# Optimization experiments

Hardware: AMD Instinct MI355X
Metric: run time of the kernel (lower is better)

Reference implementation:

```python
import jax, jax.numpy as jnp
import numpy as np

STRIDE = 32
WINDOW = 16


def setup_inputs() -> dict:
    key = jax.random.key(0)
    kq, kk, kv = jax.random.split(key, 3)
    B, H, S, D = 1, 16, 2048, 64
    q = jax.random.normal(kq, (B, H, S, D), dtype=jnp.float32)
    k = jax.random.normal(kk, (B, H, S, D), dtype=jnp.float32)
    v = jax.random.normal(kv, (B, H, S, D), dtype=jnp.float32)
    return {"q": q, "k": k, "v": v}


def _strided_attention(q, k, v, stride=STRIDE, w=WINDOW):
    b, h, n, d = q.shape
    scale = jnp.asarray(1.0 / np.sqrt(d), dtype=q.dtype)

    # strided (global) tokens: indices 0, stride, 2*stride, ...  [S_str]
    str_idx = jnp.arange(0, n, stride)
    k_str = k[:, :, str_idx, :]  # [b,h,S_str,d]
    v_str = v[:, :, str_idx, :]

    # local window gather: token i attends to j in [i-w, i+w]  (L = 2w+1 slots)
    offs = jnp.arange(-w, w + 1)                      # [L]
    pos = jnp.arange(n)[:, None] + offs[None, :]      # [n, L]
    local_valid = (pos >= 0) & (pos < n)              # [n, L]
    pos_c = jnp.clip(pos, 0, n - 1)
    k_loc = k[:, :, pos_c, :]                         # [b,h,n,L,d]
    v_loc = v[:, :, pos_c, :]                         # [b,h,n,L,d]

    # In the original, strided keys are concatenated ONLY when start > 0,
    # i.e. when i > w (since strided_indices[0] == 0 is inside the window
    # whenever start == 0). Duplicates (strided token inside the local
    # window) are intentionally kept, matching torch.cat semantics.
    use_str = jnp.arange(n) > w                       # [n]

    sc_loc = jnp.einsum('bhnd,bhnld->bhnl', q, k_loc) * scale
    sc_loc = jnp.where(local_valid[None, None], sc_loc, -jnp.inf)
    sc_str = jnp.einsum('bhnd,bhsd->bhns', q, k_str) * scale
    sc_str = jnp.where(use_str[None, None, :, None], sc_str, -jnp.inf)

    L = offs.shape[0]
    attn = jax.nn.softmax(jnp.concatenate([sc_loc, sc_str], axis=-1), axis=-1)
    attn = jnp.nan_to_num(attn, nan=0.0)
    a_loc, a_str = attn[..., :L], attn[..., L:]

    out = jnp.einsum('bhnl,bhnld->bhnd', a_loc, v_loc) \
        + jnp.einsum('bhns,bhsd->bhnd', a_str, v_str)
    return out


def reference(q, k, v):
    return _strided_attention(q, k, v)
```

## Files before the change

kernel.cpp:

```cpp
#include <hip/hip_runtime.h>
#include <math.h>


typedef __attribute__((ext_vector_type(8))) short bf16x8;
typedef __attribute__((ext_vector_type(4))) float f32x4;

constexpr int H = 16, S = 2048, D = 64, W = 16;
constexpr int QB      = 64;
constexpr int NLOCROW = 96;
constexpr int NROWS   = 160;
constexpr int NT      = 10;
constexpr float SCALE = 0.125f;

constexpr int QSTR = 72;
constexpr int VSTR = 168;
constexpr int QHI  = 0;
constexpr int QLO  = QHI + QB * QSTR;
constexpr int KHI  = QLO + QB * QSTR;
constexpr int KLO  = KHI + NROWS * QSTR;
constexpr int VTB  = KHI;
constexpr int PB   = VTB + D * VSTR;
constexpr int LDS_U = KLO + NROWS * QSTR;

__device__ __forceinline__ ushort f2bf(float x) {
    union { float f; unsigned u; } t; t.f = x;
    unsigned r = t.u + 0x7fffu + ((t.u >> 16) & 1u);
    return (ushort)(r >> 16);
}
__device__ __forceinline__ float bf2f(ushort b) {
    union { float f; unsigned u; } t; t.u = ((unsigned)b) << 16;
    return t.f;
}
__device__ __forceinline__ int rowpos(int r, int n0) {
    if (r < NLOCROW) {
        int p = n0 - W + r;
        return p < 0 ? 0 : (p > S - 1 ? S - 1 : p);
    }
    return (r - NLOCROW) * 32;
}

__global__ __launch_bounds__(256, 2) void strided_attn_mfma(
    const float* __restrict__ q,
    const float* __restrict__ k,
    const float* __restrict__ v,
    float* __restrict__ out)
{
    __shared__ ushort lds[LDS_U];

    const int tid  = threadIdx.x;
    const int w    = tid >> 6;
    const int lane = tid & 63;
    const int h    = blockIdx.x >> 5;
    const int n0   = (blockIdx.x & 31) << 6;

    const float* __restrict__ qh = q + (size_t)(h * S) * D;
    const float* __restrict__ kh = k + (size_t)(h * S) * D;
    const float* __restrict__ vh = v + (size_t)(h * S) * D;

    const int ntask = (tid < 128) ? 3 : 2;
    float4 vreg[3][4];
#pragma unroll
    for (int tt = 0; tt < 3; ++tt) {
        if (tt < ntask) {
            const int t2 = tid + (tt << 8);
            const int rp = t2 % 80, ch = t2 / 80;
            const int p0 = rowpos(2 * rp,     n0);
            const int p1 = rowpos(2 * rp + 1, n0);
            const float* s0 = vh + (size_t)p0 * D + ch * 8;
            const float* s1 = vh + (size_t)p1 * D + ch * 8;
            vreg[tt][0] = *(const float4*)s0;
            vreg[tt][1] = *(const float4*)(s0 + 4);
            vreg[tt][2] = *(const float4*)s1;
            vreg[tt][3] = *(const float4*)(s1 + 4);
        }
    }

    for (int t = tid; t < 1792; t += 256) {
        int row, ch, dhi, dlo;
        const float* src;
        if (t < 512) {
            row = t >> 3; ch = t & 7;
            src = qh + (size_t)(n0 + row) * D + ch * 8;
            dhi = QHI + row * QSTR + ch * 8;
            dlo = QLO + row * QSTR + ch * 8;
        } else {
            const int u = t - 512;
            row = u >> 3; ch = u & 7;
            src = kh + (size_t)rowpos(row, n0) * D + ch * 8;
            dhi = KHI + row * QSTR + ch * 8;
            dlo = KLO + row * QSTR + ch * 8;
        }
        const float4 a = *(const float4*)src;
        const float4 b = *(const float4*)(src + 4);
        const float xs[8] = {a.x, a.y, a.z, a.w, b.x, b.y, b.z, b.w};
        union { bf16x8 v; ushort u[8]; } hi, lo;
#pragma unroll
        for (int j = 0; j < 8; ++j) {
            const ushort hb = f2bf(xs[j]);
            hi.u[j] = hb;
            lo.u[j] = f2bf(xs[j] - bf2f(hb));
        }
        *(bf16x8*)&lds[dhi] = hi.v;
        *(bf16x8*)&lds[dlo] = lo.v;
    }
    __syncthreads();

    const int band = w * 16;
    const int c = lane & 15;
    const int g = lane >> 4;
    const int abase = (band + c) * QSTR + g * 8;
    const bf16x8 aH0 = *(bf16x8*)&lds[QHI + abase];
    const bf16x8 aH1 = *(bf16x8*)&lds[QHI + abase + 32];
    const bf16x8 aL0 = *(bf16x8*)&lds[QLO + abase];
    const bf16x8 aL1 = *(bf16x8*)&lds[QLO + abase + 32];

    f32x4 acc[NT];
#pragma unroll
    for (int t = 0; t < NT; ++t) acc[t] = (f32x4){0.f, 0.f, 0.f, 0.f};

#pragma unroll
    for (int t = 0; t < NT; ++t) {
        const int kb = (t * 16 + c) * QSTR + g * 8;
        const bf16x8 bH0 = *(bf16x8*)&lds[KHI + kb];
        const bf16x8 bH1 = *(bf16x8*)&lds[KHI + kb + 32];
        const bf16x8 bL0 = *(bf16x8*)&lds[KLO + kb];
        const bf16x8 bL1 = *(bf16x8*)&lds[KLO + kb + 32];
        f32x4 a4 = acc[t];
        a4 = __builtin_amdgcn_mfma_f32_16x16x32_bf16(aH0, bH0, a4, 0, 0, 0);
        a4 = __builtin_amdgcn_mfma_f32_16x16x32_bf16(aH1, bH1, a4, 0, 0, 0);
        a4 = __builtin_amdgcn_mfma_f32_16x16x32_bf16(aL0, bH0, a4, 0, 0, 0);
        a4 = __builtin_amdgcn_mfma_f32_16x16x32_bf16(aL1, bH1, a4, 0, 0, 0);
        a4 = __builtin_amdgcn_mfma_f32_16x16x32_bf16(aH0, bL0, a4, 0, 0, 0);
        a4 = __builtin_amdgcn_mfma_f32_16x16x32_bf16(aH1, bL1, a4, 0, 0, 0);
        acc[t] = a4;
    }

    float pw[4][NT];
    float linv[4];
#pragma unroll
    for (int i = 0; i < 4; ++i) {
        const int qi = band + g * 4 + i;
        const int n  = n0 + qi;
        float s[NT];
#pragma unroll
        for (int t = 0; t < 6; ++t) {
            const int j = t * 16 + c;
            const bool ok = ((unsigned)(j - qi) <= 32u) &&
                            ((unsigned)(n0 - W + j) < (unsigned)S);
            s[t] = ok ? acc[t][i] * SCALE : -INFINITY;
        }
        const bool us = n > W;
#pragma unroll
        for (int t = 6; t < NT; ++t)
            s[t] = us ? acc[t][i] * SCALE : -INFINITY;

        float m = s[0];
#pragma unroll
        for (int t = 1; t < NT; ++t) m = fmaxf(m, s[t]);
        m = fmaxf(m, __shfl_xor(m, 1));
        m = fmaxf(m, __shfl_xor(m, 2));
        m = fmaxf(m, __shfl_xor(m, 4));
        m = fmaxf(m, __shfl_xor(m, 8));

        float l = 0.f;
#pragma unroll
        for (int t = 0; t < NT; ++t) { pw[i][t] = __expf(s[t] - m); l += pw[i][t]; }
        l += __shfl_xor(l, 1);
        l += __shfl_xor(l, 2);
        l += __shfl_xor(l, 4);
        l += __shfl_xor(l, 8);
        linv[i] = 1.0f / l;
    }

    __syncthreads();

#pragma unroll
    for (int i = 0; i < 4; ++i) {
        const int pb = PB + (band + g * 4 + i) * VSTR + c;
#pragma unroll
        for (int t = 0; t < NT; ++t) lds[pb + t * 16] = f2bf(pw[i][t]);
    }

#pragma unroll
    for (int tt = 0; tt < 3; ++tt) {
        if (tt < ntask) {
            const int t2 = tid + (tt << 8);
            const int rp = t2 % 80, ch = t2 / 80;
            const float r0[8] = {vreg[tt][0].x, vreg[tt][0].y, vreg[tt][0].z, vreg[tt][0].w,
                                 vreg[tt][1].x, vreg[tt][1].y, vreg[tt][1].z, vreg[tt][1].w};
            const float r1[8] = {vreg[tt][2].x, vreg[tt][2].y, vreg[tt][2].z, vreg[tt][2].w,
                                 vreg[tt][3].x, vreg[tt][3].y, vreg[tt][3].z, vreg[tt][3].w};
#pragma unroll
            for (int j = 0; j < 8; ++j) {
                const unsigned pk = (unsigned)f2bf(r0[j]) | ((unsigned)f2bf(r1[j]) << 16);
                *(unsigned*)&lds[VTB + (ch * 8 + j) * VSTR + 2 * rp] = pk;
            }
        }
    }
    __syncthreads();

    f32x4 o[4];
#pragma unroll
    for (int dt = 0; dt < 4; ++dt) o[dt] = (f32x4){0.f, 0.f, 0.f, 0.f};

#pragma unroll
    for (int kt = 0; kt < 5; ++kt) {
        const bf16x8 pa = *(bf16x8*)&lds[PB + (band + c) * VSTR + kt * 32 + g * 8];
#pragma unroll
        for (int dt = 0; dt < 4; ++dt) {
            const bf16x8 vb = *(bf16x8*)&lds[VTB + (dt * 16 + c) * VSTR + kt * 32 + g * 8];
            o[dt] = __builtin_amdgcn_mfma_f32_16x16x32_bf16(pa, vb, o[dt], 0, 0, 0);
        }
    }

#pragma unroll
    for (int i = 0; i < 4; ++i) {
        const int n = n0 + band + g * 4 + i;
        float* op = out + ((size_t)(h * S) + n) * D + c;
#pragma unroll
        for (int dt = 0; dt < 4; ++dt) op[dt * 16] = o[dt][i] * linv[i];
    }
}

extern "C" void kernel_launch(void* const* d_in, const int* in_sizes, int n_in,
                              void* d_out, int out_size, void* d_ws, size_t ws_size,
                              hipStream_t stream) {
    (void)in_sizes; (void)n_in; (void)d_ws; (void)ws_size; (void)out_size;
    const float* q = (const float*)d_in[0];
    const float* k = (const float*)d_in[1];
    const float* v = (const float*)d_in[2];
    float* out     = (float*)d_out;

    dim3 grid(H * (S / QB));
    dim3 block(256);
    strided_attn_mfma<<<grid, block, 0, stream>>>(q, k, v, out);
}
```

Baseline: 18.41 us.

## Halve query block, split keys across warps, drop K low-part MFMAs

Query blocks shrink from 64 to 32 rows, and the four warps become a 2x2 grid: query band by key half (local versus strided). Partial softmax max and sum are merged through a small shared-memory buffer. K is stored only as bf16 hi, which drops the hi*lo correction MFMAs. The PV product is split across warps by output dimension, block IDs are swizzled, and occupancy is raised to 4 blocks per CU. In exchange there is an extra barrier, more grid blocks that reload the strided K/V rows, and lower precision for QK scores.

```diff
diff --git a/kernel.cpp b/kernel.cpp
--- a/kernel.cpp
+++ b/kernel.cpp
@@ -6,21 +6,20 @@
 typedef __attribute__((ext_vector_type(4))) float f32x4;
 
 constexpr int H = 16, S = 2048, D = 64, W = 16;
-constexpr int QB      = 64;
-constexpr int NLOCROW = 96;
-constexpr int NROWS   = 160;
-constexpr int NT      = 10;
+constexpr int QB    = 32;
+constexpr int NLOC  = 64;
+constexpr int NROWS = 128;
 constexpr float SCALE = 0.125f;
 
 constexpr int QSTR = 72;
-constexpr int VSTR = 168;
+constexpr int VSTR = 136;
 constexpr int QHI  = 0;
 constexpr int QLO  = QHI + QB * QSTR;
-constexpr int KHI  = QLO + QB * QSTR;
-constexpr int KLO  = KHI + NROWS * QSTR;
-constexpr int VTB  = KHI;
-constexpr int PB   = VTB + D * VSTR;
-constexpr int LDS_U = KLO + NROWS * QSTR;
+constexpr int KB   = QLO + QB * QSTR;
+constexpr int VTB  = 0;
+constexpr int PBF  = VTB + D * VSTR;
+constexpr int MLB  = KB + NROWS * QSTR;
+constexpr int LDS_U = MLB + 256;
 
 __device__ __forceinline__ ushort f2bf(float x) {
     union { float f; unsigned u; } t; t.f = x;
@@ -32,193 +31,203 @@
     return t.f;
 }
 __device__ __forceinline__ int rowpos(int r, int n0) {
-    if (r < NLOCROW) {
+    if (r < NLOC) {
         int p = n0 - W + r;
         return p < 0 ? 0 : (p > S - 1 ? S - 1 : p);
     }
-    return (r - NLOCROW) * 32;
-}
-
-__global__ __launch_bounds__(256, 2) void strided_attn_mfma(
+    return (r - NLOC) * 32;
+}
+
+__global__ __launch_bounds__(256, 4) void strided_attn_mfma(
     const float* __restrict__ q,
     const float* __restrict__ k,
     const float* __restrict__ v,
     float* __restrict__ out)
 {
     __shared__ ushort lds[LDS_U];
+    float* ml = (float*)&lds[MLB];
 
     const int tid  = threadIdx.x;
     const int w    = tid >> 6;
     const int lane = tid & 63;
-    const int h    = blockIdx.x >> 5;
-    const int n0   = (blockIdx.x & 31) << 6;
+    const int wq   = w >> 1;
+    const int wk   = w & 1;
+    const int bid  = blockIdx.x;
+    const int swz  = (bid & 7) * 128 + (bid >> 3);
+    const int h    = swz >> 6;
+    const int n0   = (swz & 63) << 5;
 
     const float* __restrict__ qh = q + (size_t)(h * S) * D;
     const float* __restrict__ kh = k + (size_t)(h * S) * D;
     const float* __restrict__ vh = v + (size_t)(h * S) * D;
 
-    const int ntask = (tid < 128) ? 3 : 2;
-    float4 vreg[3][4];
-#pragma unroll
-    for (int tt = 0; tt < 3; ++tt) {
-        if (tt < ntask) {
-            const int t2 = tid + (tt << 8);
-            const int rp = t2 % 80, ch = t2 / 80;
-            const int p0 = rowpos(2 * rp,     n0);
-            const int p1 = rowpos(2 * rp + 1, n0);
-            const float* s0 = vh + (size_t)p0 * D + ch * 8;
-            const float* s1 = vh + (size_t)p1 * D + ch * 8;
-            vreg[tt][0] = *(const float4*)s0;
-            vreg[tt][1] = *(const float4*)(s0 + 4);
-            vreg[tt][2] = *(const float4*)s1;
-            vreg[tt][3] = *(const float4*)(s1 + 4);
-        }
-    }
-
-    for (int t = tid; t < 1792; t += 256) {
-        int row, ch, dhi, dlo;
-        const float* src;
-        if (t < 512) {
-            row = t >> 3; ch = t & 7;
-            src = qh + (size_t)(n0 + row) * D + ch * 8;
-            dhi = QHI + row * QSTR + ch * 8;
-            dlo = QLO + row * QSTR + ch * 8;
+    float4 vreg[2][4];
+#pragma unroll
+    for (int tt = 0; tt < 2; ++tt) {
+        const int tau = tid + (tt << 8);
+        const int rp = tau & 63, ch = tau >> 6;
+        const int p0 = rowpos(2 * rp,     n0);
+        const int p1 = rowpos(2 * rp + 1, n0);
+        const float* s0 = vh + (size_t)p0 * D + ch * 8;
+        const float* s1 = vh + (size_t)p1 * D + ch * 8;
+        vreg[tt][0] = *(const float4*)s0;
+        vreg[tt][1] = *(const float4*)(s0 + 4);
+        vreg[tt][2] = *(const float4*)s1;
+        vreg[tt][3] = *(const float4*)(s1 + 4);
+    }
+
+    for (int t = tid; t < 1280; t += 256) {
+        if (t < 256) {
+            const int row = t >> 3, ch = t & 7;
+            const float* src = qh + (size_t)(n0 + row) * D + ch * 8;
+            const float4 a = *(const float4*)src;
+            const float4 b = *(const float4*)(src + 4);
+            const float xs[8] = {a.x, a.y, a.z, a.w, b.x, b.y, b.z, b.w};
+            union { bf16x8 v; ushort u[8]; } hi, lo;
+#pragma unroll
+            for (int j = 0; j < 8; ++j) {
+                const ushort hb = f2bf(xs[j]);
+                hi.u[j] = hb;
+                lo.u[j] = f2bf(xs[j] - bf2f(hb));
+            }
+            *(bf16x8*)&lds[QHI + row * QSTR + ch * 8] = hi.v;
+            *(bf16x8*)&lds[QLO + row * QSTR + ch * 8] = lo.v;
         } else {
-            const int u = t - 512;
-            row = u >> 3; ch = u & 7;
-            src = kh + (size_t)rowpos(row, n0) * D + ch * 8;
-            dhi = KHI + row * QSTR + ch * 8;
-            dlo = KLO + row * QSTR + ch * 8;
-        }
-        const float4 a = *(const float4*)src;
-        const float4 b = *(const float4*)(src + 4);
-        const float xs[8] = {a.x, a.y, a.z, a.w, b.x, b.y, b.z, b.w};
-        union { bf16x8 v; ushort u[8]; } hi, lo;
-#pragma unroll
-        for (int j = 0; j < 8; ++j) {
-            const ushort hb = f2bf(xs[j]);
-            hi.u[j] = hb;
-            lo.u[j] = f2bf(xs[j] - bf2f(hb));
-        }
-        *(bf16x8*)&lds[dhi] = hi.v;
-        *(bf16x8*)&lds[dlo] = lo.v;
+            const int u = t - 256;
+            const int row = u >> 3, ch = u & 7;
+            const float* src = kh + (size_t)rowpos(row, n0) * D + ch * 8;
+            const float4 a = *(const float4*)src;
+            const float4 b = *(const float4*)(src + 4);
+            const float xs[8] = {a.x, a.y, a.z, a.w, b.x, b.y, b.z, b.w};
+            union { bf16x8 v; ushort u[8]; } hi;
+#pragma unroll
+            for (int j = 0; j < 8; ++j) hi.u[j] = f2bf(xs[j]);
+            *(bf16x8*)&lds[KB + row * QSTR + ch * 8] = hi.v;
+        }
     }
     __syncthreads();
 
-    const int band = w * 16;
     const int c = lane & 15;
     const int g = lane >> 4;
-    const int abase = (band + c) * QSTR + g * 8;
+    const int abase = (wq * 16 + c) * QSTR + g * 8;
     const bf16x8 aH0 = *(bf16x8*)&lds[QHI + abase];
     const bf16x8 aH1 = *(bf16x8*)&lds[QHI + abase + 32];
     const bf16x8 aL0 = *(bf16x8*)&lds[QLO + abase];
     const bf16x8 aL1 = *(bf16x8*)&lds[QLO + abase + 32];
 
-    f32x4 acc[NT];
-#pragma unroll
-    for (int t = 0; t < NT; ++t) acc[t] = (f32x4){0.f, 0.f, 0.f, 0.f};
-
-#pragma unroll
-    for (int t = 0; t < NT; ++t) {
-        const int kb = (t * 16 + c) * QSTR + g * 8;
-        const bf16x8 bH0 = *(bf16x8*)&lds[KHI + kb];
-        const bf16x8 bH1 = *(bf16x8*)&lds[KHI + kb + 32];
-        const bf16x8 bL0 = *(bf16x8*)&lds[KLO + kb];
-        const bf16x8 bL1 = *(bf16x8*)&lds[KLO + kb + 32];
+    f32x4 acc[4];
+#pragma unroll
+    for (int t = 0; t < 4; ++t) acc[t] = (f32x4){0.f, 0.f, 0.f, 0.f};
+#pragma unroll
+    for (int t = 0; t < 4; ++t) {
+        const int kb = KB + (wk * 64 + t * 16 + c) * QSTR + g * 8;
+        const bf16x8 b0 = *(bf16x8*)&lds[kb];
+        const bf16x8 b1 = *(bf16x8*)&lds[kb + 32];
         f32x4 a4 = acc[t];
-        a4 = __builtin_amdgcn_mfma_f32_16x16x32_bf16(aH0, bH0, a4, 0, 0, 0);
-        a4 = __builtin_amdgcn_mfma_f32_16x16x32_bf16(aH1, bH1, a4, 0, 0, 0);
-        a4 = __builtin_amdgcn_mfma_f32_16x16x32_bf16(aL0, bH0, a4, 0, 0, 0);
-        a4 = __builtin_amdgcn_mfma_f32_16x16x32_bf16(aL1, bH1, a4, 0, 0, 0);
-        a4 = __builtin_amdgcn_mfma_f32_16x16x32_bf16(aH0, bL0, a4, 0, 0, 0);
-        a4 = __builtin_amdgcn_mfma_f32_16x16x32_bf16(aH1, bL1, a4, 0, 0, 0);
+        a4 = __builtin_amdgcn_mfma_f32_16x16x32_bf16(aH0, b0, a4, 0, 0, 0);
+        a4 = __builtin_amdgcn_mfma_f32_16x16x32_bf16(aH1, b1, a4, 0, 0, 0);
+        a4 = __builtin_amdgcn_mfma_f32_16x16x32_bf16(aL0, b0, a4, 0, 0, 0);
+        a4 = __builtin_amdgcn_mfma_f32_16x16x32_bf16(aL1, b1, a4, 0, 0, 0);
         acc[t] = a4;
     }
 
-    float pw[4][NT];
-    float linv[4];
+    float sv[4][4];
+    float mw[4], lw[4];
 #pragma unroll
     for (int i = 0; i < 4; ++i) {
-        const int qi = band + g * 4 + i;
+        const int qi = wq * 16 + g * 4 + i;
         const int n  = n0 + qi;
-        float s[NT];
-#pragma unroll
-        for (int t = 0; t < 6; ++t) {
-            const int j = t * 16 + c;
-            const bool ok = ((unsigned)(j - qi) <= 32u) &&
-                            ((unsigned)(n0 - W + j) < (unsigned)S);
-            s[t] = ok ? acc[t][i] * SCALE : -INFINITY;
-        }
-        const bool us = n > W;
-#pragma unroll
-        for (int t = 6; t < NT; ++t)
-            s[t] = us ? acc[t][i] * SCALE : -INFINITY;
-
-        float m = s[0];
-#pragma unroll
-        for (int t = 1; t < NT; ++t) m = fmaxf(m, s[t]);
+        if (wk == 0) {
+#pragma unroll
+            for (int t = 0; t < 4; ++t) {
+                const int j = t * 16 + c;
+                const bool ok = ((unsigned)(j - qi) <= 32u) &&
+                                ((unsigned)(n0 - W + j) < (unsigned)S);
+                sv[i][t] = ok ? acc[t][i] * SCALE : -INFINITY;
+            }
+        } else {
+            const bool us = n > W;
+#pragma unroll
+            for (int t = 0; t < 4; ++t)
+                sv[i][t] = us ? acc[t][i] * SCALE : -INFINITY;
+        }
+        float m = fmaxf(fmaxf(sv[i][0], sv[i][1]), fmaxf(sv[i][2], sv[i][3]));
         m = fmaxf(m, __shfl_xor(m, 1));
         m = fmaxf(m, __shfl_xor(m, 2));
         m = fmaxf(m, __shfl_xor(m, 4));
         m = fmaxf(m, __shfl_xor(m, 8));
-
+        mw[i] = m;
+        const float ms = fmaxf(m, -1e30f);
         float l = 0.f;
 #pragma unroll
-        for (int t = 0; t < NT; ++t) { pw[i][t] = __expf(s[t] - m); l += pw[i][t]; }
+        for (int t = 0; t < 4; ++t) l += __expf(sv[i][t] - ms);
         l += __shfl_xor(l, 1);
         l += __shfl_xor(l, 2);
         l += __shfl_xor(l, 4);
         l += __shfl_xor(l, 8);
+        lw[i] = l;
+    }
+    if (c == 0) {
+#pragma unroll
+        for (int i = 0; i < 4; ++i) {
+            const int qi = wq * 16 + g * 4 + i;
+            ml[qi * 4 + wk * 2 + 0] = mw[i];
+            ml[qi * 4 + wk * 2 + 1] = lw[i];
+        }
+    }
+    __syncthreads();
+
+    float linv[4];
+#pragma unroll
+    for (int i = 0; i < 4; ++i) {
+        const int qi = wq * 16 + g * 4 + i;
+        const float m0 = ml[qi * 4 + 0], l0 = ml[qi * 4 + 1];
+        const float m1 = ml[qi * 4 + 2], l1 = ml[qi * 4 + 3];
+        const float m  = fmaxf(m0, m1);
+        const float l  = l0 * __expf(fmaxf(m0, -1e30f) - m)
+                       + l1 * __expf(fmaxf(m1, -1e30f) - m);
         linv[i] = 1.0f / l;
-    }
-
+        const int pb = PBF + qi * VSTR + wk * 64;
+#pragma unroll
+        for (int t = 0; t < 4; ++t)
+            lds[pb + t * 16 + c] = f2bf(__expf(sv[i][t] - m));
+    }
+
+#pragma unroll
+    for (int tt = 0; tt < 2; ++tt) {
+        const int tau = tid + (tt << 8);
+        const int rp = tau & 63, ch = tau >> 6;
+        const float r0[8] = {vreg[tt][0].x, vreg[tt][0].y, vreg[tt][0].z, vreg[tt][0].w,
+                             vreg[tt][1].x, vreg[tt][1].y, vreg[tt][1].z, vreg[tt][1].w};
+        const float r1[8] = {vreg[tt][2].x, vreg[tt][2].y, vreg[tt][2].z, vreg[tt][2].w,
+                             vreg[tt][3].x, vreg[tt][3].y, vreg[tt][3].z, vreg[tt][3].w};
+#pragma unroll
+        for (int j = 0; j < 8; ++j) {
+            const unsigned pk = (unsigned)f2bf(r0[j]) | ((unsigned)f2bf(r1[j]) << 16);
+            *(unsigned*)&lds[VTB + (ch * 8 + j) * VSTR + 2 * rp] = pk;
+        }
+    }
     __syncthreads();
 
+    f32x4 o[2];
+    o[0] = (f32x4){0.f, 0.f, 0.f, 0.f};
+    o[1] = (f32x4){0.f, 0.f, 0.f, 0.f};
+#pragma unroll
+    for (int kt = 0; kt < 4; ++kt) {
+        const bf16x8 pa = *(bf16x8*)&lds[PBF + (wq * 16 + c) * VSTR + kt * 32 + g * 8];
+#pragma unroll
+        for (int dt = 0; dt < 2; ++dt) {
+            const bf16x8 vb = *(bf16x8*)&lds[VTB + (wk * 32 + dt * 16 + c) * VSTR + kt * 32 + g * 8];
+            o[dt] = __builtin_amdgcn_mfma_f32_16x16x32_bf16(pa, vb, o[dt], 0, 0, 0);
+        }
+    }
+
 #pragma unroll
     for (int i = 0; i < 4; ++i) {
-        const int pb = PB + (band + g * 4 + i) * VSTR + c;
-#pragma unroll
-        for (int t = 0; t < NT; ++t) lds[pb + t * 16] = f2bf(pw[i][t]);
-    }
-
-#pragma unroll
-    for (int tt = 0; tt < 3; ++tt) {
-        if (tt < ntask) {
-            const int t2 = tid + (tt << 8);
-            const int rp = t2 % 80, ch = t2 / 80;
-            const float r0[8] = {vreg[tt][0].x, vreg[tt][0].y, vreg[tt][0].z, vreg[tt][0].w,
-                                 vreg[tt][1].x, vreg[tt][1].y, vreg[tt][1].z, vreg[tt][1].w};
-            const float r1[8] = {vreg[tt][2].x, vreg[tt][2].y, vreg[tt][2].z, vreg[tt][2].w,
-                                 vreg[tt][3].x, vreg[tt][3].y, vreg[tt][3].z, vreg[tt][3].w};
-#pragma unroll
-            for (int j = 0; j < 8; ++j) {
-                const unsigned pk = (unsigned)f2bf(r0[j]) | ((unsigned)f2bf(r1[j]) << 16);
-                *(unsigned*)&lds[VTB + (ch * 8 + j) * VSTR + 2 * rp] = pk;
-            }
-        }
-    }
-    __syncthreads();
-
-    f32x4 o[4];
-#pragma unroll
-    for (int dt = 0; dt < 4; ++dt) o[dt] = (f32x4){0.f, 0.f, 0.f, 0.f};
-
-#pragma unroll
-    for (int kt = 0; kt < 5; ++kt) {
-        const bf16x8 pa = *(bf16x8*)&lds[PB + (band + c) * VSTR + kt * 32 + g * 8];
-#pragma unroll
-        for (int dt = 0; dt < 4; ++dt) {
-            const bf16x8 vb = *(bf16x8*)&lds[VTB + (dt * 16 + c) * VSTR + kt * 32 + g * 8];
-            o[dt] = __builtin_amdgcn_mfma_f32_16x16x32_bf16(pa, vb, o[dt], 0, 0, 0);
-        }
-    }
-
-#pragma unroll
-    for (int i = 0; i < 4; ++i) {
-        const int n = n0 + band + g * 4 + i;
-        float* op = out + ((size_t)(h * S) + n) * D + c;
-#pragma unroll
-        for (int dt = 0; dt < 4; ++dt) op[dt * 16] = o[dt][i] * linv[i];
+        const int n = n0 + wq * 16 + g * 4 + i;
+        float* op = out + ((size_t)(h * S) + n) * D + wk * 32 + c;
+        op[0]  = o[0][i] * linv[i];
+        op[16] = o[1][i] * linv[i];
     }
 }
 
```

Result: faster. 17.88 us (-2.9%).

## Transpose QK^T so P stays in registers; drop K low split; swizzle blocks

Applied to the files above, without the earlier changes.

Computes S^T = K·Q^T so that each lane holds one query's scores. The softmax reduction then needs only two cross-lane shuffles, and the normalized probabilities can be packed directly into MFMA A-operands in registers instead of going through an LDS P buffer. The V^T layout is permuted so it matches that register ordering. The K low-precision split term is dropped, which cuts QK MFMAs from 6 to 4 per tile and halves K LDS storage, at some cost in score accuracy. A block-index swizzle is also added, and V conversion to bf16 is done before the barrier.

```diff
diff --git a/kernel.cpp b/kernel.cpp
--- a/kernel.cpp
+++ b/kernel.cpp
@@ -6,21 +6,19 @@
 typedef __attribute__((ext_vector_type(4))) float f32x4;
 
 constexpr int H = 16, S = 2048, D = 64, W = 16;
-constexpr int QB      = 64;
-constexpr int NLOCROW = 96;
-constexpr int NROWS   = 160;
-constexpr int NT      = 10;
+constexpr int QB    = 64;
+constexpr int NLOC  = 96;
+constexpr int NROWS = 160;
+constexpr int NT    = 10;
 constexpr float SCALE = 0.125f;
 
 constexpr int QSTR = 72;
 constexpr int VSTR = 168;
 constexpr int QHI  = 0;
 constexpr int QLO  = QHI + QB * QSTR;
-constexpr int KHI  = QLO + QB * QSTR;
-constexpr int KLO  = KHI + NROWS * QSTR;
-constexpr int VTB  = KHI;
-constexpr int PB   = VTB + D * VSTR;
-constexpr int LDS_U = KLO + NROWS * QSTR;
+constexpr int KB   = QLO + QB * QSTR;
+constexpr int VTB  = 0;
+constexpr int LDS_U = KB + NROWS * QSTR;
 
 __device__ __forceinline__ ushort f2bf(float x) {
     union { float f; unsigned u; } t; t.f = x;
@@ -31,12 +29,15 @@
     union { float f; unsigned u; } t; t.u = ((unsigned)b) << 16;
     return t.f;
 }
+__device__ __forceinline__ unsigned pk2(float a, float b) {
+    return (unsigned)f2bf(a) | ((unsigned)f2bf(b) << 16);
+}
 __device__ __forceinline__ int rowpos(int r, int n0) {
-    if (r < NLOCROW) {
+    if (r < NLOC) {
         int p = n0 - W + r;
         return p < 0 ? 0 : (p > S - 1 ? S - 1 : p);
     }
-    return (r - NLOCROW) * 32;
+    return (r - NLOC) * 32;
 }
 
 __global__ __launch_bounds__(256, 2) void strided_attn_mfma(
@@ -50,8 +51,12 @@
     const int tid  = threadIdx.x;
     const int w    = tid >> 6;
     const int lane = tid & 63;
-    const int h    = blockIdx.x >> 5;
-    const int n0   = (blockIdx.x & 31) << 6;
+    const int c    = lane & 15;
+    const int g    = lane >> 4;
+    const int bid  = blockIdx.x;
+    const int swz  = (bid & 7) * 64 + (bid >> 3);
+    const int h    = swz >> 5;
+    const int n0   = (swz & 31) << 6;
 
     const float* __restrict__ qh = q + (size_t)(h * S) * D;
     const float* __restrict__ kh = k + (size_t)(h * S) * D;
@@ -62,12 +67,10 @@
 #pragma unroll
     for (int tt = 0; tt < 3; ++tt) {
         if (tt < ntask) {
-            const int t2 = tid + (tt << 8);
-            const int rp = t2 % 80, ch = t2 / 80;
-            const int p0 = rowpos(2 * rp,     n0);
-            const int p1 = rowpos(2 * rp + 1, n0);
-            const float* s0 = vh + (size_t)p0 * D + ch * 8;
-            const float* s1 = vh + (size_t)p1 * D + ch * 8;
+            const int tau = tid + (tt << 8);
+            const int rp = tau % 80, ch = tau / 80;
+            const float* s0 = vh + (size_t)rowpos(2 * rp,     n0) * D + ch * 8;
+            const float* s1 = vh + (size_t)rowpos(2 * rp + 1, n0) * D + ch * 8;
             vreg[tt][0] = *(const float4*)s0;
             vreg[tt][1] = *(const float4*)(s0 + 4);
             vreg[tt][2] = *(const float4*)s1;
@@ -76,149 +79,153 @@
     }
 
     for (int t = tid; t < 1792; t += 256) {
-        int row, ch, dhi, dlo;
-        const float* src;
         if (t < 512) {
-            row = t >> 3; ch = t & 7;
-            src = qh + (size_t)(n0 + row) * D + ch * 8;
-            dhi = QHI + row * QSTR + ch * 8;
-            dlo = QLO + row * QSTR + ch * 8;
+            const int row = t >> 3, ch = t & 7;
+            const float* src = qh + (size_t)(n0 + row) * D + ch * 8;
+            const float4 a = *(const float4*)src;
+            const float4 b = *(const float4*)(src + 4);
+            const float xs[8] = {a.x, a.y, a.z, a.w, b.x, b.y, b.z, b.w};
+            union { bf16x8 v; ushort u[8]; } hi, lo;
+#pragma unroll
+            for (int j = 0; j < 8; ++j) {
+                const ushort hb = f2bf(xs[j]);
+                hi.u[j] = hb;
+                lo.u[j] = f2bf(xs[j] - bf2f(hb));
+            }
+            *(bf16x8*)&lds[QHI + row * QSTR + ch * 8] = hi.v;
+            *(bf16x8*)&lds[QLO + row * QSTR + ch * 8] = lo.v;
         } else {
             const int u = t - 512;
-            row = u >> 3; ch = u & 7;
-            src = kh + (size_t)rowpos(row, n0) * D + ch * 8;
-            dhi = KHI + row * QSTR + ch * 8;
-            dlo = KLO + row * QSTR + ch * 8;
-        }
-        const float4 a = *(const float4*)src;
-        const float4 b = *(const float4*)(src + 4);
-        const float xs[8] = {a.x, a.y, a.z, a.w, b.x, b.y, b.z, b.w};
-        union { bf16x8 v; ushort u[8]; } hi, lo;
-#pragma unroll
-        for (int j = 0; j < 8; ++j) {
-            const ushort hb = f2bf(xs[j]);
-            hi.u[j] = hb;
-            lo.u[j] = f2bf(xs[j] - bf2f(hb));
-        }
-        *(bf16x8*)&lds[dhi] = hi.v;
-        *(bf16x8*)&lds[dlo] = lo.v;
-    }
-    __syncthreads();
-
-    const int band = w * 16;
-    const int c = lane & 15;
-    const int g = lane >> 4;
-    const int abase = (band + c) * QSTR + g * 8;
-    const bf16x8 aH0 = *(bf16x8*)&lds[QHI + abase];
-    const bf16x8 aH1 = *(bf16x8*)&lds[QHI + abase + 32];
-    const bf16x8 aL0 = *(bf16x8*)&lds[QLO + abase];
-    const bf16x8 aL1 = *(bf16x8*)&lds[QLO + abase + 32];
-
-    f32x4 acc[NT];
-#pragma unroll
-    for (int t = 0; t < NT; ++t) acc[t] = (f32x4){0.f, 0.f, 0.f, 0.f};
-
-#pragma unroll
-    for (int t = 0; t < NT; ++t) {
-        const int kb = (t * 16 + c) * QSTR + g * 8;
-        const bf16x8 bH0 = *(bf16x8*)&lds[KHI + kb];
-        const bf16x8 bH1 = *(bf16x8*)&lds[KHI + kb + 32];
-        const bf16x8 bL0 = *(bf16x8*)&lds[KLO + kb];
-        const bf16x8 bL1 = *(bf16x8*)&lds[KLO + kb + 32];
-        f32x4 a4 = acc[t];
-        a4 = __builtin_amdgcn_mfma_f32_16x16x32_bf16(aH0, bH0, a4, 0, 0, 0);
-        a4 = __builtin_amdgcn_mfma_f32_16x16x32_bf16(aH1, bH1, a4, 0, 0, 0);
-        a4 = __builtin_amdgcn_mfma_f32_16x16x32_bf16(aL0, bH0, a4, 0, 0, 0);
-        a4 = __builtin_amdgcn_mfma_f32_16x16x32_bf16(aL1, bH1, a4, 0, 0, 0);
-        a4 = __builtin_amdgcn_mfma_f32_16x16x32_bf16(aH0, bL0, a4, 0, 0, 0);
-        a4 = __builtin_amdgcn_mfma_f32_16x16x32_bf16(aH1, bL1, a4, 0, 0, 0);
-        acc[t] = a4;
-    }
-
-    float pw[4][NT];
-    float linv[4];
-#pragma unroll
-    for (int i = 0; i < 4; ++i) {
-        const int qi = band + g * 4 + i;
-        const int n  = n0 + qi;
-        float s[NT];
-#pragma unroll
-        for (int t = 0; t < 6; ++t) {
-            const int j = t * 16 + c;
-            const bool ok = ((unsigned)(j - qi) <= 32u) &&
-                            ((unsigned)(n0 - W + j) < (unsigned)S);
-            s[t] = ok ? acc[t][i] * SCALE : -INFINITY;
-        }
-        const bool us = n > W;
-#pragma unroll
-        for (int t = 6; t < NT; ++t)
-            s[t] = us ? acc[t][i] * SCALE : -INFINITY;
-
-        float m = s[0];
-#pragma unroll
-        for (int t = 1; t < NT; ++t) m = fmaxf(m, s[t]);
-        m = fmaxf(m, __shfl_xor(m, 1));
-        m = fmaxf(m, __shfl_xor(m, 2));
-        m = fmaxf(m, __shfl_xor(m, 4));
-        m = fmaxf(m, __shfl_xor(m, 8));
-
-        float l = 0.f;
-#pragma unroll
-        for (int t = 0; t < NT; ++t) { pw[i][t] = __expf(s[t] - m); l += pw[i][t]; }
-        l += __shfl_xor(l, 1);
-        l += __shfl_xor(l, 2);
-        l += __shfl_xor(l, 4);
-        l += __shfl_xor(l, 8);
-        linv[i] = 1.0f / l;
-    }
-
-    __syncthreads();
-
-#pragma unroll
-    for (int i = 0; i < 4; ++i) {
-        const int pb = PB + (band + g * 4 + i) * VSTR + c;
-#pragma unroll
-        for (int t = 0; t < NT; ++t) lds[pb + t * 16] = f2bf(pw[i][t]);
-    }
-
+            const int row = u >> 3, ch = u & 7;
+            const float* src = kh + (size_t)rowpos(row, n0) * D + ch * 8;
+            const float4 a = *(const float4*)src;
+            const float4 b = *(const float4*)(src + 4);
+            const float xs[8] = {a.x, a.y, a.z, a.w, b.x, b.y, b.z, b.w};
+            union { bf16x8 v; ushort u[8]; } hi;
+#pragma unroll
+            for (int j = 0; j < 8; ++j) hi.u[j] = f2bf(xs[j]);
+            *(bf16x8*)&lds[KB + row * QSTR + ch * 8] = hi.v;
+        }
+    }
+
+    unsigned vpk[3][8];
 #pragma unroll
     for (int tt = 0; tt < 3; ++tt) {
         if (tt < ntask) {
-            const int t2 = tid + (tt << 8);
-            const int rp = t2 % 80, ch = t2 / 80;
             const float r0[8] = {vreg[tt][0].x, vreg[tt][0].y, vreg[tt][0].z, vreg[tt][0].w,
                                  vreg[tt][1].x, vreg[tt][1].y, vreg[tt][1].z, vreg[tt][1].w};
             const float r1[8] = {vreg[tt][2].x, vreg[tt][2].y, vreg[tt][2].z, vreg[tt][2].w,
                                  vreg[tt][3].x, vreg[tt][3].y, vreg[tt][3].z, vreg[tt][3].w};
 #pragma unroll
-            for (int j = 0; j < 8; ++j) {
-                const unsigned pk = (unsigned)f2bf(r0[j]) | ((unsigned)f2bf(r1[j]) << 16);
-                *(unsigned*)&lds[VTB + (ch * 8 + j) * VSTR + 2 * rp] = pk;
-            }
+            for (int j = 0; j < 8; ++j) vpk[tt][j] = pk2(r0[j], r1[j]);
         }
     }
     __syncthreads();
 
+    const int qb = w * 16;
+    const int qi = qb + c;
+    const int nq = n0 + qi;
+    const int qa = (qb + c) * QSTR + g * 8;
+    const bf16x8 bQH0 = *(bf16x8*)&lds[QHI + qa];
+    const bf16x8 bQH1 = *(bf16x8*)&lds[QHI + qa + 32];
+    const bf16x8 bQL0 = *(bf16x8*)&lds[QLO + qa];
+    const bf16x8 bQL1 = *(bf16x8*)&lds[QLO + qa + 32];
+
+    f32x4 acc[NT];
+#pragma unroll
+    for (int t = 0; t < NT; ++t) acc[t] = (f32x4){0.f, 0.f, 0.f, 0.f};
+#pragma unroll
+    for (int t = 0; t < NT; ++t) {
+        const int kb = KB + (t * 16 + c) * QSTR + g * 8;
+        const bf16x8 a0 = *(bf16x8*)&lds[kb];
+        const bf16x8 a1 = *(bf16x8*)&lds[kb + 32];
+        f32x4 a4 = acc[t];
+        a4 = __builtin_amdgcn_mfma_f32_16x16x32_bf16(a0, bQH0, a4, 0, 0, 0);
+        a4 = __builtin_amdgcn_mfma_f32_16x16x32_bf16(a1, bQH1, a4, 0, 0, 0);
+        a4 = __builtin_amdgcn_mfma_f32_16x16x32_bf16(a0, bQL0, a4, 0, 0, 0);
+        a4 = __builtin_amdgcn_mfma_f32_16x16x32_bf16(a1, bQL1, a4, 0, 0, 0);
+        acc[t] = a4;
+    }
+
+    float p[NT][4];
+#pragma unroll
+    for (int t = 0; t < 6; ++t) {
+#pragma unroll
+        for (int i = 0; i < 4; ++i) {
+            const int j = t * 16 + 4 * g + i;
+            const bool ok = ((unsigned)(j - qi) <= 32u) &&
+                            ((unsigned)(n0 - W + j) < (unsigned)S);
+            p[t][i] = ok ? acc[t][i] * SCALE : -INFINITY;
+        }
+    }
+    const bool us = nq > W;
+#pragma unroll
+    for (int t = 6; t < NT; ++t)
+#pragma unroll
+        for (int i = 0; i < 4; ++i)
+            p[t][i] = us ? acc[t][i] * SCALE : -INFINITY;
+
+    float m = -INFINITY;
+#pragma unroll
+    for (int t = 0; t < NT; ++t)
+#pragma unroll
+        for (int i = 0; i < 4; ++i) m = fmaxf(m, p[t][i]);
+    m = fmaxf(m, __shfl_xor(m, 16));
+    m = fmaxf(m, __shfl_xor(m, 32));
+
+    float l = 0.f;
+#pragma unroll
+    for (int t = 0; t < NT; ++t)
+#pragma unroll
+        for (int i = 0; i < 4; ++i) { p[t][i] = __expf(p[t][i] - m); l += p[t][i]; }
+    l += __shfl_xor(l, 16);
+    l += __shfl_xor(l, 32);
+    const float inv = 1.0f / l;
+
+    union { bf16x8 v; unsigned u[4]; } pa[5];
+#pragma unroll
+    for (int kt = 0; kt < 5; ++kt) {
+        pa[kt].u[0] = pk2(p[2 * kt][0] * inv,     p[2 * kt][1] * inv);
+        pa[kt].u[1] = pk2(p[2 * kt][2] * inv,     p[2 * kt][3] * inv);
+        pa[kt].u[2] = pk2(p[2 * kt + 1][0] * inv, p[2 * kt + 1][1] * inv);
+        pa[kt].u[3] = pk2(p[2 * kt + 1][2] * inv, p[2 * kt + 1][3] * inv);
+    }
+
+    __syncthreads();
+
+#pragma unroll
+    for (int tt = 0; tt < 3; ++tt) {
+        if (tt < ntask) {
+            const int tau = tid + (tt << 8);
+            const int rp = tau % 80, ch = tau / 80;
+            const int kk = 2 * rp;
+            const int kt = kk >> 5, rem = kk & 31;
+            const int slot = kt * 32 + ((rem >> 2) & 3) * 8 + (rem >> 4) * 4 + (rem & 3);
+#pragma unroll
+            for (int j = 0; j < 8; ++j)
+                *(unsigned*)&lds[VTB + (ch * 8 + j) * VSTR + slot] = vpk[tt][j];
+        }
+    }
+    __syncthreads();
+
     f32x4 o[4];
 #pragma unroll
     for (int dt = 0; dt < 4; ++dt) o[dt] = (f32x4){0.f, 0.f, 0.f, 0.f};
-
 #pragma unroll
     for (int kt = 0; kt < 5; ++kt) {
-        const bf16x8 pa = *(bf16x8*)&lds[PB + (band + c) * VSTR + kt * 32 + g * 8];
 #pragma unroll
         for (int dt = 0; dt < 4; ++dt) {
             const bf16x8 vb = *(bf16x8*)&lds[VTB + (dt * 16 + c) * VSTR + kt * 32 + g * 8];
-            o[dt] = __builtin_amdgcn_mfma_f32_16x16x32_bf16(pa, vb, o[dt], 0, 0, 0);
+            o[dt] = __builtin_amdgcn_mfma_f32_16x16x32_bf16(pa[kt].v, vb, o[dt], 0, 0, 0);
         }
     }
 
 #pragma unroll
     for (int i = 0; i < 4; ++i) {
-        const int n = n0 + band + g * 4 + i;
+        const int n = n0 + qb + 4 * g + i;
         float* op = out + ((size_t)(h * S) + n) * D + c;
 #pragma unroll
-        for (int dt = 0; dt < 4; ++dt) op[dt * 16] = o[dt][i] * linv[i];
+        for (int dt = 0; dt < 4; ++dt) op[dt * 16] = o[dt][i];
     }
 }
 
```

Result: faster. 15.33 us (-16.8%).
